# Performance work log

Hardware: AMD Instinct MI355X
Metric: run time of the kernel (lower is better)

## Reference

```python
import jax, jax.numpy as jnp
import numpy as np

N = 200000
C = 128
VOX = 0.05
EPS = 1e-5
OFFSETS = np.array([[dz, dy, dx] for dz in (-1, 0, 1) for dy in (-1, 0, 1) for dx in (-1, 0, 1)], dtype=np.int64)


def setup_inputs() -> dict:
    key = jax.random.key(0)
    ks = jax.random.split(key, 8)
    gp = jax.random.normal(ks[0], (N, 14), jnp.float32)
    # ---- voxelization tables (int constants, computed once in numpy) ----
    pts = np.asarray(gp[:, :3], dtype=np.float64)
    vc = np.floor(pts / VOX).astype(np.int64)
    vc = vc - vc.min(axis=0)
    mx = vc.max(axis=0) + 1
    h = vc[:, 0] * mx[1] * mx[2] + vc[:, 1] * mx[2] + vc[:, 2]
    uh, inv = np.unique(h, return_inverse=True)
    M = int(uh.shape[0])
    vcoord = np.zeros((M, 3), np.int64)
    vcoord[inv] = vc  # coords identical for same hash
    nbr_idx = np.zeros((M, 27), np.int32)
    nbr_mask = np.zeros((M, 27), np.float32)
    for o in range(27):
        nc = vcoord + OFFSETS[o]
        inb = (nc >= 0).all(1) & (nc < mx).all(1)
        nh = nc[:, 0] * mx[1] * mx[2] + nc[:, 1] * mx[2] + nc[:, 2]
        pos = np.clip(np.searchsorted(uh, nh), 0, M - 1)
        found = inb & (uh[pos] == nh)
        nbr_idx[:, o] = np.where(found, pos, 0)
        nbr_mask[:, o] = found.astype(np.float32)
    s = 0.05
    return {
        'gaussian_params': gp,
        'w_enc': jax.random.normal(ks[1], (14, C), jnp.float32) * s,
        'b_enc': jnp.zeros((C,), jnp.float32),
        'ln_g': jnp.ones((C,), jnp.float32),
        'ln_b': jnp.zeros((C,), jnp.float32),
        'conv_w': jax.random.normal(ks[2], (4, 27, C, C), jnp.float32) * s,
        'bn_g': jnp.ones((4, C), jnp.float32),
        'bn_b': jnp.zeros((4, C), jnp.float32),
        'w1': jax.random.normal(ks[3], (C, C // 2), jnp.float32) * s,
        'b1': jnp.zeros((C // 2,), jnp.float32),
        'w2': jax.random.normal(ks[4], (C // 2, 14), jnp.float32) * s,
        'b2': jnp.zeros((14,), jnp.float32),
        'nbr_mask': jnp.asarray(nbr_mask),
        'inv_idx': jnp.asarray(inv.astype(np.int32)),
        'nbr_idx': jnp.asarray(nbr_idx),
        'num_voxels': M,
    }


def _bn(x, g, b):
    m = x.mean(0)
    v = x.var(0)
    return (x - m) * jax.lax.rsqrt(v + EPS) * g + b


def _subm(x, W, nbr_idx, nbr_mask):
    # submanifold 3x3x3 conv: sum over 27 offsets of masked neighbor gather @ W[o]
    out = jnp.zeros_like(x)
    for o in range(27):
        out = out + (x[nbr_idx[:, o]] * nbr_mask[:, o:o + 1]) @ W[o]
    return out


def _forward(gp, w_enc, b_enc, ln_g, ln_b, conv_w, bn_g, bn_b, w1, b1, w2, b2, nbr_mask, inv_idx, nbr_idx, num_voxels):
    # input encoder: Linear -> LayerNorm -> ReLU
    f = gp @ w_enc + b_enc
    mu = f.mean(-1, keepdims=True)
    var = f.var(-1, keepdims=True)
    f = jax.nn.relu((f - mu) * jax.lax.rsqrt(var + EPS) * ln_g + ln_b)
    # points -> voxels: segment mean (the op the torch code did with a Python loop)
    cnt = jax.ops.segment_sum(jnp.ones((gp.shape[0],), f.dtype), inv_idx, num_segments=num_voxels)
    x = jax.ops.segment_sum(f, inv_idx, num_segments=num_voxels) / cnt[:, None]
    # 2 residual sparse conv blocks (BN uses batch stats, training-mode forward)
    for blk in range(2):
        idn = x
        out = _subm(x, conv_w[2 * blk], nbr_idx, nbr_mask)
        out = jax.nn.relu(_bn(out, bn_g[2 * blk], bn_b[2 * blk]))
        out = _subm(out, conv_w[2 * blk + 1], nbr_idx, nbr_mask)
        x = jax.nn.relu(_bn(out, bn_g[2 * blk + 1], bn_b[2 * blk + 1]) + idn)
    # voxels -> points, output head, residual add
    pf = x[inv_idx]
    delta = jax.nn.relu(pf @ w1 + b1) @ w2 + b2
    return gp[:, :14] + delta


def reference(gaussian_params, w_enc, b_enc, ln_g, ln_b, conv_w, bn_g, bn_b, w1, b1, w2, b2, nbr_mask, inv_idx, nbr_idx, num_voxels):
    return _forward(gaussian_params, w_enc, b_enc, ln_g, ln_b, conv_w, bn_g, bn_b, w1, b1, w2, b2, nbr_mask, inv_idx, nbr_idx, num_voxels)
```

## Files before the change

kernel.cpp:

```cpp
#include <hip/hip_runtime.h>

typedef __bf16 bf16x8 __attribute__((ext_vector_type(8)));
typedef float f32x16 __attribute__((ext_vector_type(16)));

#define LN_EPS 1e-5f
#define AS1 __attribute__((address_space(1)))
#define AS3 __attribute__((address_space(3)))

__device__ __forceinline__ unsigned f2bf_rne(float f) {
    unsigned x = __float_as_uint(f);
    return (x + 0x7fffu + ((x >> 16) & 1u)) >> 16;
}

__device__ __forceinline__ float bf2f(unsigned short u) {
    return __uint_as_float((unsigned)u << 16);
}

__global__ void pack_w_kernel(const float* __restrict__ cw, unsigned short* __restrict__ Wp, int E) {
    int idx = blockIdx.x * 256 + threadIdx.x;
    if (idx >= E) return;
    float v = cw[idx];
    int n  = idx & 127;
    int c  = (idx >> 7) & 127;
    int oc = idx >> 14;
    Wp[oc * 16384 + (c >> 3) * 1024 + n * 8 + (c & 7)] = (unsigned short)f2bf_rne(v);
}

__global__ void pack_w1_kernel(const float* __restrict__ w1, unsigned short* __restrict__ Wp1) {
    int idx = blockIdx.x * 256 + threadIdx.x;
    if (idx >= 8192) return;
    int k = idx >> 6, n = idx & 63;
    Wp1[(k >> 3) * 512 + n * 8 + (k & 7)] = (unsigned short)f2bf_rne(w1[k * 64 + n]);
}

__global__ void prep_nbr_kernel(const int* __restrict__ nbr_idx, const float* __restrict__ nbr_mask,
                                int* __restrict__ T, unsigned* __restrict__ act, int M) {
    int m = blockIdx.x * 256 + threadIdx.x;
    if (m >= M) return;
    unsigned bits = 0;
#pragma unroll
    for (int o = 0; o < 27; ++o) {
        bool f = nbr_mask[m * 27 + o] != 0.f;
        int g = f ? nbr_idx[m * 27 + o] : M;
        T[o * M + m] = g;
        bits |= (f ? 1u : 0u) << o;
    }
    atomicOr(&act[m >> 7], bits);
}

__global__ void count_kernel(const int* __restrict__ inv, int* __restrict__ cnt, int N) {
    int p = blockIdx.x * 256 + threadIdx.x;
    if (p < N) atomicAdd(&cnt[inv[p]], 1);
}

__global__ void scan1_kernel(const int* __restrict__ cnt, int* __restrict__ starts,
                             int* __restrict__ partials, int M) {
    __shared__ int sdata[256];
    int t = threadIdx.x;
    int base = blockIdx.x * 1024;
    int v[4], tot = 0;
#pragma unroll
    for (int j = 0; j < 4; ++j) {
        int idx = base + t * 4 + j;
        v[j] = idx < M ? cnt[idx] : 0;
        tot += v[j];
    }
    sdata[t] = tot;
    __syncthreads();
    for (int off = 1; off < 256; off <<= 1) {
        int x = (t >= off) ? sdata[t - off] : 0;
        __syncthreads();
        sdata[t] += x;
        __syncthreads();
    }
    int run = sdata[t] - tot;
#pragma unroll
    for (int j = 0; j < 4; ++j) {
        int idx = base + t * 4 + j;
        if (idx < M) starts[idx] = run;
        run += v[j];
    }
    if (t == 255) partials[blockIdx.x] = run;
}

__global__ void scan2_kernel(int* __restrict__ partials, int nb) {
    __shared__ int sdata[256];
    int t = threadIdx.x;
    int v[4], tot = 0;
#pragma unroll
    for (int j = 0; j < 4; ++j) {
        int idx = t * 4 + j;
        v[j] = idx < nb ? partials[idx] : 0;
        tot += v[j];
    }
    sdata[t] = tot;
    __syncthreads();
    for (int off = 1; off < 256; off <<= 1) {
        int x = (t >= off) ? sdata[t - off] : 0;
        __syncthreads();
        sdata[t] += x;
        __syncthreads();
    }
    int run = sdata[t] - tot;
#pragma unroll
    for (int j = 0; j < 4; ++j) {
        int idx = t * 4 + j;
        if (idx < nb) partials[idx] = run;
        run += v[j];
    }
}

__global__ void fill_kernel(const int* __restrict__ inv, const int* __restrict__ starts,
                            const int* __restrict__ partials, int* __restrict__ tmp,
                            int* __restrict__ plist, int N) {
    int p = blockIdx.x * 256 + threadIdx.x;
    if (p >= N) return;
    int v = inv[p];
    int slot = atomicAdd(&tmp[v], 1);
    plist[starts[v] + partials[v >> 10] + slot] = p;
}

__global__ __launch_bounds__(256) void vox_encode_kernel(
    const float* __restrict__ gp, const float* __restrict__ w_enc,
    const float* __restrict__ b_enc, const float* __restrict__ ln_g,
    const float* __restrict__ ln_b, const int* __restrict__ starts,
    const int* __restrict__ partials, const int* __restrict__ cnt,
    const int* __restrict__ plist, unsigned short* __restrict__ A, int M)
{
    int v = blockIdx.x * 4 + (threadIdx.x >> 6);
    int lane = threadIdx.x & 63;
    if (v >= M) return;
    int st = starts[v] + partials[v >> 10];
    int n = cnt[v];
    const float2* w2p = (const float2*)w_enc;
    float2 be = ((const float2*)b_enc)[lane];
    float2 lg = ((const float2*)ln_g)[lane];
    float2 lb = ((const float2*)ln_b)[lane];
    float a0 = 0.f, a1 = 0.f;
    for (int i = 0; i < n; ++i) {
        int p = plist[st + i];
        float f0 = be.x, f1 = be.y;
#pragma unroll
        for (int k = 0; k < 14; ++k) {
            float gv = gp[p * 14 + k];
            float2 wv = w2p[k * 64 + lane];
            f0 = fmaf(gv, wv.x, f0);
            f1 = fmaf(gv, wv.y, f1);
        }
        float s = f0 + f1;
#pragma unroll
        for (int off = 32; off; off >>= 1) s += __shfl_xor(s, off);
        float mean = s * 0.0078125f;
        float d0 = f0 - mean, d1 = f1 - mean;
        float var = d0 * d0 + d1 * d1;
#pragma unroll
        for (int off = 32; off; off >>= 1) var += __shfl_xor(var, off);
        float rs = rsqrtf(var * 0.0078125f + LN_EPS);
        float h0 = d0 * rs * lg.x + lb.x;
        float h1 = d1 * rs * lg.y + lb.y;
        a0 += h0 > 0.f ? h0 : 0.f;
        a1 += h1 > 0.f ? h1 : 0.f;
    }
    float r = 1.f / (float)n;
    ((unsigned*)A)[v * 64 + lane] = f2bf_rne(a0 * r) | (f2bf_rne(a1 * r) << 16);
}

__global__ __launch_bounds__(256, 2) void subm_conv_kernel(
    const unsigned short* __restrict__ xin,
    const unsigned short* __restrict__ Wp,
    const int* __restrict__ T, const unsigned* __restrict__ act,
    float* __restrict__ yout, float* __restrict__ stats, int M)
{
    __shared__ uint4 Ws[2][2048];

    const int tid = threadIdx.x;
    const int lane = tid & 63;
    const int w = tid >> 6;
    const int m0 = blockIdx.x * 128;
    const int rw = w * 32;
    const int q = lane >> 5;
    const int l31 = lane & 31;
    int myrow = m0 + rw + l31;
    if (myrow >= M) myrow = M - 1;

    f32x16 acc[4];
#pragma unroll
    for (int t = 0; t < 4; ++t)
#pragma unroll
        for (int r = 0; r < 16; ++r) acc[t][r] = 0.f;

    const uint4* xin4 = (const uint4*)xin;
    unsigned amask = act[blockIdx.x];
    int o_cur = __ffs(amask) - 1;
    amask &= amask - 1;
    int buf = 0;
    uint4 afA[8], afB[8];

    {
        const uint4* WpO4 = (const uint4*)Wp + o_cur * 2048;
#pragma unroll
        for (int rep = 0; rep < 8; ++rep)
            __builtin_amdgcn_global_load_lds(
                (const AS1 unsigned int*)(WpO4 + rep * 256 + tid),
                (AS3 unsigned int*)(&Ws[0][rep * 256 + w * 64]), 16, 0, 0);
        int g = T[o_cur * M + myrow];
#pragma unroll
        for (int j = 0; j < 8; ++j) afA[j] = xin4[g * 16 + 2 * j + q];
    }

    auto conv_step = [&](uint4 (&afC)[8], uint4 (&afN)[8]) {
        int o_next = -1;
        if (amask) { o_next = __ffs(amask) - 1; amask &= amask - 1; }
        __syncthreads();
        if (o_next >= 0) {
            const uint4* WpO4 = (const uint4*)Wp + o_next * 2048;
#pragma unroll
            for (int rep = 0; rep < 8; ++rep)
                __builtin_amdgcn_global_load_lds(
                    (const AS1 unsigned int*)(WpO4 + rep * 256 + tid),
                    (AS3 unsigned int*)(&Ws[buf ^ 1][rep * 256 + w * 64]), 16, 0, 0);
            int g = T[o_next * M + myrow];
#pragma unroll
            for (int j = 0; j < 8; ++j) afN[j] = xin4[g * 16 + 2 * j + q];
        }
        const bf16x8* wsb = (const bf16x8*)&Ws[buf][0];
#pragma unroll
        for (int ks = 0; ks < 8; ++ks) {
            int kb = (ks << 1) | q;
            bf16x8 a = *(const bf16x8*)&afC[ks];
#pragma unroll
            for (int tn = 0; tn < 4; ++tn) {
                bf16x8 b = wsb[kb * 128 + tn * 32 + l31];
                acc[tn] = __builtin_amdgcn_mfma_f32_32x32x16_bf16(a, b, acc[tn], 0, 0, 0);
            }
        }
        buf ^= 1;
        o_cur = o_next;
    };

    while (o_cur >= 0) {
        conv_step(afA, afB);
        if (o_cur < 0) break;
        conv_step(afB, afA);
    }

#pragma unroll
    for (int tn = 0; tn < 4; ++tn) {
        int col = tn * 32 + l31;
        float s = 0.f, sq = 0.f;
#pragma unroll
        for (int r = 0; r < 16; ++r) {
            int rloc = (r & 3) + 8 * (r >> 2) + 4 * q + rw;
            int grow = m0 + rloc;
            float v = acc[tn][r];
            if (grow < M) {
                yout[grow * 128 + col] = v;
                s += v; sq += v * v;
            }
        }
        s += __shfl_xor(s, 32);
        sq += __shfl_xor(sq, 32);
        if (lane < 32) {
            atomicAdd(&stats[col], s);
            atomicAdd(&stats[128 + col], sq);
        }
    }
}

__global__ void bn_relu_kernel(const float* __restrict__ y, const float* __restrict__ stats,
                               const float* __restrict__ g, const float* __restrict__ b,
                               unsigned short* __restrict__ out, int total4, float invM) {
    int idx = blockIdx.x * 256 + threadIdx.x;
    if (idx >= total4) return;
    int e0 = idx * 4;
    int c0 = e0 & 127;
    float4 yv = *(const float4*)(y + e0);
    float h[4];
    const float* yp = (const float*)&yv;
#pragma unroll
    for (int j = 0; j < 4; ++j) {
        int c = c0 + j;
        float mean = stats[c] * invM;
        float var = stats[128 + c] * invM - mean * mean;
        float sc = g[c] * rsqrtf(var + LN_EPS);
        float sh = b[c] - mean * sc;
        float vv = yp[j] * sc + sh;
        h[j] = vv > 0.f ? vv : 0.f;
    }
    uint2 pk;
    pk.x = f2bf_rne(h[0]) | (f2bf_rne(h[1]) << 16);
    pk.y = f2bf_rne(h[2]) | (f2bf_rne(h[3]) << 16);
    *(uint2*)(out + e0) = pk;
}

__global__ void bn_relu_res_kernel(const float* __restrict__ y, const float* __restrict__ stats,
                                   const float* __restrict__ g, const float* __restrict__ b,
                                   const unsigned short* __restrict__ idn,
                                   unsigned short* __restrict__ out, int total4, float invM) {
    int idx = blockIdx.x * 256 + threadIdx.x;
    if (idx >= total4) return;
    int e0 = idx * 4;
    int c0 = e0 & 127;
    float4 yv = *(const float4*)(y + e0);
    uint2 iv = *(const uint2*)(idn + e0);
    float id[4];
    id[0] = __uint_as_float(iv.x << 16);
    id[1] = __uint_as_float(iv.x & 0xffff0000u);
    id[2] = __uint_as_float(iv.y << 16);
    id[3] = __uint_as_float(iv.y & 0xffff0000u);
    float h[4];
    const float* yp = (const float*)&yv;
#pragma unroll
    for (int j = 0; j < 4; ++j) {
        int c = c0 + j;
        float mean = stats[c] * invM;
        float var = stats[128 + c] * invM - mean * mean;
        float sc = g[c] * rsqrtf(var + LN_EPS);
        float sh = b[c] - mean * sc;
        float vv = yp[j] * sc + sh + id[j];
        h[j] = vv > 0.f ? vv : 0.f;
    }
    uint2 pk;
    pk.x = f2bf_rne(h[0]) | (f2bf_rne(h[1]) << 16);
    pk.y = f2bf_rne(h[2]) | (f2bf_rne(h[3]) << 16);
    *(uint2*)(out + e0) = pk;
}

__global__ __launch_bounds__(256) void head_vox_kernel(
    const unsigned short* __restrict__ A,
    const unsigned short* __restrict__ Wp1,
    const float* __restrict__ b1, const float* __restrict__ w2,
    const float* __restrict__ b2, float* __restrict__ Dv, int M)
{
    __shared__ uint4 W1s[1024];
    __shared__ unsigned short Hs[8192];
    __shared__ float w2s[896];

    const int tid = threadIdx.x;
    const int lane = tid & 63;
    const int w = tid >> 6;
    const int m0 = blockIdx.x * 128;
    const int rw = w * 32;
    const int q = lane >> 5;
    const int l31 = lane & 31;
    int myrow = m0 + rw + l31;
    if (myrow > M) myrow = M;

#pragma unroll
    for (int rep = 0; rep < 4; ++rep) {
        __builtin_amdgcn_global_load_lds(
            (const AS1 unsigned int*)((const uint4*)Wp1 + rep * 256 + tid),
            (AS3 unsigned int*)(W1s + rep * 256 + w * 64), 16, 0, 0);
    }
    for (int i = tid; i < 896; i += 256) w2s[i] = w2[i];

    const uint4* xin4 = (const uint4*)A;
    uint4 af[8];
#pragma unroll
    for (int j = 0; j < 8; ++j) af[j] = xin4[myrow * 16 + 2 * j + q];

    f32x16 acc[2];
#pragma unroll
    for (int t = 0; t < 2; ++t)
#pragma unroll
        for (int r = 0; r < 16; ++r) acc[t][r] = 0.f;

    __syncthreads();

#pragma unroll
    for (int ks = 0; ks < 8; ++ks) {
        int kb = (ks << 1) | q;
        bf16x8 a = *(const bf16x8*)&af[ks];
#pragma unroll
        for (int tn = 0; tn < 2; ++tn) {
            bf16x8 b = ((const bf16x8*)W1s)[kb * 64 + tn * 32 + l31];
            acc[tn] = __builtin_amdgcn_mfma_f32_32x32x16_bf16(a, b, acc[tn], 0, 0, 0);
        }
    }

#pragma unroll
    for (int tn = 0; tn < 2; ++tn) {
        int col = tn * 32 + l31;
        float bias = b1[col];
        int ch = col >> 3, ce = col & 7;
#pragma unroll
        for (int r = 0; r < 16; ++r) {
            int rloc = (r & 3) + 8 * (r >> 2) + 4 * q + rw;
            float v = acc[tn][r] + bias;
            v = v > 0.f ? v : 0.f;
            Hs[rloc * 64 + (ch ^ (rloc & 7)) * 8 + ce] = (unsigned short)f2bf_rne(v);
        }
    }
    __syncthreads();

    int r2 = tid >> 1;
    int c0 = (tid & 1) * 7;
    float o[7];
#pragma unroll
    for (int j = 0; j < 7; ++j) o[j] = b2[c0 + j];
#pragma unroll
    for (int c = 0; c < 8; ++c) {
        bf16x8 hv = ((const bf16x8*)Hs)[r2 * 8 + (c ^ (r2 & 7))];
#pragma unroll
        for (int e = 0; e < 8; ++e) {
            float h = bf2f(((const unsigned short*)&hv)[e]);
            int k = c * 8 + e;
#pragma unroll
            for (int j = 0; j < 7; ++j) o[j] = fmaf(h, w2s[k * 14 + c0 + j], o[j]);
        }
    }
    int grow = m0 + r2;
    if (grow < M) {
#pragma unroll
        for (int j = 0; j < 7; ++j) Dv[grow * 14 + c0 + j] = o[j];
    }
}

__global__ void head_scatter_kernel(const float* __restrict__ gp, const float* __restrict__ Dv,
                                    const int* __restrict__ inv_idx, float* __restrict__ out, int N) {
    int p = blockIdx.x * 256 + threadIdx.x;
    if (p >= N) return;
    int vx = inv_idx[p];
#pragma unroll
    for (int c = 0; c < 14; ++c) out[p * 14 + c] = gp[p * 14 + c] + Dv[vx * 14 + c];
}

extern "C" void kernel_launch(void* const* d_in, const int* in_sizes, int n_in,
                              void* d_out, int out_size, void* d_ws, size_t ws_size,
                              hipStream_t stream) {
    const float* gp       = (const float*)d_in[0];
    const float* w_enc    = (const float*)d_in[1];
    const float* b_enc    = (const float*)d_in[2];
    const float* ln_g     = (const float*)d_in[3];
    const float* ln_b     = (const float*)d_in[4];
    const float* conv_w   = (const float*)d_in[5];
    const float* bn_g     = (const float*)d_in[6];
    const float* bn_b     = (const float*)d_in[7];
    const float* w1       = (const float*)d_in[8];
    const float* b1       = (const float*)d_in[9];
    const float* w2       = (const float*)d_in[10];
    const float* b2       = (const float*)d_in[11];
    const float* nbr_mask = (const float*)d_in[12];
    const int*   inv_idx  = (const int*)d_in[13];
    const int*   nbr_idx  = (const int*)d_in[14];

    const int N = in_sizes[0] / 14;
    const int M = in_sizes[12] / 27;
    const int ntiles128 = (M + 127) / 128;
    const int nb = (M + 1023) / 1024;

    char* ws = (char*)d_ws;
    size_t off = 0;
    unsigned short* Wp  = (unsigned short*)(ws + off); off += (size_t)4 * 27 * 16384 * 2;
    unsigned short* Wp1 = (unsigned short*)(ws + off); off += 8192 * 2;
    unsigned short* A   = (unsigned short*)(ws + off); off += (size_t)(M + 1) * 128 * 2;
    unsigned short* H   = (unsigned short*)(ws + off); off += (size_t)(M + 1) * 128 * 2;
    float* Yraw  = (float*)(ws + off); off += (size_t)M * 128 * 4;
    int* T       = (int*)(ws + off); off += (size_t)27 * M * 4;
    int* starts  = (int*)(ws + off); off += (size_t)M * 4;
    int* plist   = (int*)(ws + off); off += (size_t)N * 4;
    int* partials= (int*)(ws + off); off += 1024 * 4;
    size_t zoff = off;
    int* cnt     = (int*)(ws + off); off += (size_t)M * 4;
    int* tmp     = (int*)(ws + off); off += (size_t)M * 4;
    float* stats = (float*)(ws + off); off += 4 * 256 * 4;
    unsigned* act= (unsigned*)(ws + off); off += (size_t)ntiles128 * 4;
    size_t zbytes = off - zoff;
    float* Dv = Yraw;

    hipMemsetAsync(cnt, 0, zbytes, stream);
    hipMemsetAsync(A + (size_t)M * 128, 0, 256, stream);
    hipMemsetAsync(H + (size_t)M * 128, 0, 256, stream);

    const int E = 4 * 27 * 128 * 128;
    pack_w_kernel<<<(E + 255) / 256, 256, 0, stream>>>(conv_w, Wp, E);
    pack_w1_kernel<<<32, 256, 0, stream>>>(w1, Wp1);
    prep_nbr_kernel<<<(M + 255) / 256, 256, 0, stream>>>(nbr_idx, nbr_mask, T, act, M);

    count_kernel<<<(N + 255) / 256, 256, 0, stream>>>(inv_idx, cnt, N);
    scan1_kernel<<<nb, 256, 0, stream>>>(cnt, starts, partials, M);
    scan2_kernel<<<1, 256, 0, stream>>>(partials, nb);
    fill_kernel<<<(N + 255) / 256, 256, 0, stream>>>(inv_idx, starts, partials, tmp, plist, N);
    vox_encode_kernel<<<(M + 3) / 4, 256, 0, stream>>>(
        gp, w_enc, b_enc, ln_g, ln_b, starts, partials, cnt, plist, A, M);

    const int total4 = M * 32;
    const float invM = 1.f / (float)M;
    for (int blk = 0; blk < 2; ++blk) {
        int c0 = 2 * blk, c1 = 2 * blk + 1;
        subm_conv_kernel<<<ntiles128, 256, 0, stream>>>(
            A, Wp + (size_t)c0 * 27 * 16384, T, act, Yraw, stats + c0 * 256, M);
        bn_relu_kernel<<<(total4 + 255) / 256, 256, 0, stream>>>(
            Yraw, stats + c0 * 256, bn_g + c0 * 128, bn_b + c0 * 128, H, total4, invM);
        subm_conv_kernel<<<ntiles128, 256, 0, stream>>>(
            H, Wp + (size_t)c1 * 27 * 16384, T, act, Yraw, stats + c1 * 256, M);
        bn_relu_res_kernel<<<(total4 + 255) / 256, 256, 0, stream>>>(
            Yraw, stats + c1 * 256, bn_g + c1 * 128, bn_b + c1 * 128, A, A, total4, invM);
    }
    head_vox_kernel<<<ntiles128, 256, 0, stream>>>(A, Wp1, b1, w2, b2, Dv, M);
    head_scatter_kernel<<<(N + 255) / 256, 256, 0, stream>>>(gp, Dv, inv_idx, (float*)d_out, N);
}
```

Baseline: 1.551 ms.

## Deepen sparse-conv prefetch pipeline and remap tile order across blocks

The submanifold conv kernel now prefetches neighbour activation gathers two offsets ahead using three register buffers, while weights stay double-buffered in LDS. Explicit vmcnt waits plus raw barriers replace __syncthreads, so only the loads that are needed are drained before each barrier. Block indices are also permuted so that consecutive blocks handle tiles strided across the voxel range, which is meant to spread work and cache traffic. The extra register buffer raises VGPR pressure and may hurt occupancy, and the hand-coded waitcnt encodings have to match how the compiler orders the loads.

```diff
diff --git a/kernel.cpp b/kernel.cpp
--- a/kernel.cpp
+++ b/kernel.cpp
@@ -15,6 +15,10 @@
 __device__ __forceinline__ float bf2f(unsigned short u) {
     return __uint_as_float((unsigned)u << 16);
 }
+
+#define WAITCNT_VM0   0x0070
+#define WAITCNT_VM8   0x0078
+#define WAITCNT_VM16  0x4070
 
 __global__ void pack_w_kernel(const float* __restrict__ cw, unsigned short* __restrict__ Wp, int E) {
     int idx = blockIdx.x * 256 + threadIdx.x;
@@ -176,7 +180,13 @@
     const int tid = threadIdx.x;
     const int lane = tid & 63;
     const int w = tid >> 6;
-    const int m0 = blockIdx.x * 128;
+
+    int nt = gridDim.x;
+    int b = blockIdx.x;
+    int Q = nt >> 3;
+    int tile = (b < (Q << 3)) ? ((b & 7) * Q + (b >> 3)) : b;
+
+    const int m0 = tile * 128;
     const int rw = w * 32;
     const int q = lane >> 5;
     const int l31 = lane & 31;
@@ -190,39 +200,49 @@
         for (int r = 0; r < 16; ++r) acc[t][r] = 0.f;
 
     const uint4* xin4 = (const uint4*)xin;
-    unsigned amask = act[blockIdx.x];
-    int o_cur = __ffs(amask) - 1;
-    amask &= amask - 1;
+    unsigned amask = act[tile];
+
+    auto pop = [&]() -> int {
+        if (!amask) return -1;
+        int o = __ffs(amask) - 1;
+        amask &= amask - 1;
+        return o;
+    };
+
+    int cur = pop();
+    int n1 = pop();
+    int n2 = pop();
     int buf = 0;
-    uint4 afA[8], afB[8];
-
-    {
-        const uint4* WpO4 = (const uint4*)Wp + o_cur * 2048;
+    uint4 af0[8], af1[8], af2[8];
+
+    auto stageW = [&](int o, int bsel) {
+        const uint4* WpO4 = (const uint4*)Wp + o * 2048;
 #pragma unroll
         for (int rep = 0; rep < 8; ++rep)
             __builtin_amdgcn_global_load_lds(
                 (const AS1 unsigned int*)(WpO4 + rep * 256 + tid),
-                (AS3 unsigned int*)(&Ws[0][rep * 256 + w * 64]), 16, 0, 0);
-        int g = T[o_cur * M + myrow];
-#pragma unroll
-        for (int j = 0; j < 8; ++j) afA[j] = xin4[g * 16 + 2 * j + q];
-    }
-
-    auto conv_step = [&](uint4 (&afC)[8], uint4 (&afN)[8]) {
-        int o_next = -1;
-        if (amask) { o_next = __ffs(amask) - 1; amask &= amask - 1; }
-        __syncthreads();
-        if (o_next >= 0) {
-            const uint4* WpO4 = (const uint4*)Wp + o_next * 2048;
-#pragma unroll
-            for (int rep = 0; rep < 8; ++rep)
-                __builtin_amdgcn_global_load_lds(
-                    (const AS1 unsigned int*)(WpO4 + rep * 256 + tid),
-                    (AS3 unsigned int*)(&Ws[buf ^ 1][rep * 256 + w * 64]), 16, 0, 0);
-            int g = T[o_next * M + myrow];
-#pragma unroll
-            for (int j = 0; j < 8; ++j) afN[j] = xin4[g * 16 + 2 * j + q];
-        }
+                (AS3 unsigned int*)(&Ws[bsel][rep * 256 + w * 64]), 16, 0, 0);
+    };
+    auto gatherA = [&](int o, uint4 (&af)[8]) {
+        int g = T[o * M + myrow];
+#pragma unroll
+        for (int j = 0; j < 8; ++j) af[j] = xin4[g * 16 + 2 * j + q];
+    };
+
+    stageW(cur, 0);
+    gatherA(cur, af0);
+    if (n1 >= 0) {
+        gatherA(n1, af1);
+        __builtin_amdgcn_s_waitcnt(WAITCNT_VM16);
+    } else {
+        __builtin_amdgcn_s_waitcnt(WAITCNT_VM8);
+    }
+    __builtin_amdgcn_s_barrier();
+
+    auto step = [&](uint4 (&afC)[8], uint4 (&afT)[8]) {
+        if (n1 >= 0) stageW(n1, buf ^ 1);
+        bool deep = (n2 >= 0);
+        if (deep) gatherA(n2, afT);
         const bf16x8* wsb = (const bf16x8*)&Ws[buf][0];
 #pragma unroll
         for (int ks = 0; ks < 8; ++ks) {
@@ -230,18 +250,24 @@
             bf16x8 a = *(const bf16x8*)&afC[ks];
 #pragma unroll
             for (int tn = 0; tn < 4; ++tn) {
-                bf16x8 b = wsb[kb * 128 + tn * 32 + l31];
-                acc[tn] = __builtin_amdgcn_mfma_f32_32x32x16_bf16(a, b, acc[tn], 0, 0, 0);
+                bf16x8 bfr = wsb[kb * 128 + tn * 32 + l31];
+                acc[tn] = __builtin_amdgcn_mfma_f32_32x32x16_bf16(a, bfr, acc[tn], 0, 0, 0);
             }
         }
+        if (deep) {
+            __builtin_amdgcn_s_waitcnt(WAITCNT_VM8);
+        } else {
+            __builtin_amdgcn_s_waitcnt(WAITCNT_VM0);
+        }
+        __builtin_amdgcn_s_barrier();
         buf ^= 1;
-        o_cur = o_next;
+        cur = n1; n1 = n2; n2 = pop();
     };
 
-    while (o_cur >= 0) {
-        conv_step(afA, afB);
-        if (o_cur < 0) break;
-        conv_step(afB, afA);
+    while (cur >= 0) {
+        step(af0, af2); if (cur < 0) break;
+        step(af1, af0); if (cur < 0) break;
+        step(af2, af1);
     }
 
 #pragma unroll
@@ -468,9 +494,9 @@
     size_t zbytes = off - zoff;
     float* Dv = Yraw;
 
-    hipMemsetAsync(cnt, 0, zbytes, stream);
-    hipMemsetAsync(A + (size_t)M * 128, 0, 256, stream);
-    hipMemsetAsync(H + (size_t)M * 128, 0, 256, stream);
+    (void)hipMemsetAsync(cnt, 0, zbytes, stream);
+    (void)hipMemsetAsync(A + (size_t)M * 128, 0, 256, stream);
+    (void)hipMemsetAsync(H + (size_t)M * 128, 0, 256, stream);
 
     const int E = 4 * 27 * 128 * 128;
     pack_w_kernel<<<(E + 255) / 256, 256, 0, stream>>>(conv_w, Wp, E);
```

After: 1.574 ms. No clear change (+1.4%).
